# Kernel tuning notes

Measured on AMD Instinct MI355X. Metric: run time of the kernel, lower is better.

Reference implementation:

```python
import jax, jax.numpy as jnp
import numpy as np

B, S, DIM = 1, 2048, 2048
H, KVH = 32, 8
D = DIM // H  # 64


def setup_inputs() -> dict:
    key = jax.random.key(0)
    ks = jax.random.split(key, 10)
    x = jax.random.normal(ks[0], (B, S, DIM), dtype=jnp.float32)
    # RoPE frequencies: theta=10000, per LLaMA
    inv_freq = 1.0 / (10000.0 ** (np.arange(0, D, 2, dtype=np.float32) / D))  # (D/2,)
    angles = np.arange(S, dtype=np.float32)[:, None] * inv_freq[None, :]      # (S, D/2)
    freqs_cos = jnp.asarray(np.cos(angles))
    freqs_sin = jnp.asarray(np.sin(angles))
    # causal mask (1,1,S,S), 1 = keep, 0 = masked
    mask = jnp.tril(jnp.ones((S, S), dtype=jnp.int32))[None, None, :, :]
    w = 0.02
    Wq = jax.random.normal(ks[1], (DIM, H * D), dtype=jnp.float32) * w
    bq = jnp.zeros((H * D,), dtype=jnp.float32)
    Wk = jax.random.normal(ks[2], (DIM, KVH * D), dtype=jnp.float32) * w
    bk = jnp.zeros((KVH * D,), dtype=jnp.float32)
    Wv = jax.random.normal(ks[3], (DIM, KVH * D), dtype=jnp.float32) * w
    bv = jnp.zeros((KVH * D,), dtype=jnp.float32)
    Wo = jax.random.normal(ks[4], (H * D, DIM), dtype=jnp.float32) * w
    bo = jnp.zeros((DIM,), dtype=jnp.float32)
    return {"x": x, "freqs_cos": freqs_cos, "freqs_sin": freqs_sin, "mask": mask,
            "Wq": Wq, "bq": bq, "Wk": Wk, "bk": bk, "Wv": Wv, "bv": bv, "Wo": Wo, "bo": bo}


def _rope(t, cos, sin):
    # t: (B, S, h, D) with D even; rotate consecutive pairs (real form of complex mult)
    tr = t.reshape(*t.shape[:-1], -1, 2)          # (B,S,h,D/2,2)
    c = cos[None, :, None, :]                     # (1,S,1,D/2)
    s = sin[None, :, None, :]
    o0 = tr[..., 0] * c - tr[..., 1] * s
    o1 = tr[..., 0] * s + tr[..., 1] * c
    return jnp.stack([o0, o1], axis=-1).reshape(t.shape)


def reference(x, freqs_cos, freqs_sin, mask, Wq, bq, Wk, bk, Wv, bv, Wo, bo):
    b, s, dim = x.shape
    scale = 1.0 / jnp.sqrt(jnp.asarray(D, dtype=x.dtype))
    q = (x @ Wq + bq).reshape(b, s, H, D)
    k = (x @ Wk + bk).reshape(b, s, KVH, D)
    v = (x @ Wv + bv).reshape(b, s, KVH, D)
    q = _rope(q, freqs_cos, freqs_sin)
    k = _rope(k, freqs_cos, freqs_sin)
    # GQA: repeat kv heads to match query heads
    rep = H // KVH
    k = jnp.repeat(k, rep, axis=2)
    v = jnp.repeat(v, rep, axis=2)
    # to (B, H, S, D)
    q = q.transpose(0, 2, 1, 3)
    k = k.transpose(0, 2, 1, 3)
    v = v.transpose(0, 2, 1, 3)
    scores = jnp.einsum('bhqd,bhkd->bhqk', q, k) * scale   # (B,H,S,S)
    neg = jnp.asarray(jnp.finfo(scores.dtype).min, dtype=scores.dtype)
    scores = jnp.where(mask == 0, neg, scores)
    attn = jax.nn.softmax(scores, axis=-1)
    out = jnp.einsum('bhqk,bhkd->bhqd', attn, v)            # (B,H,S,D)
    out = out.transpose(0, 2, 1, 3).reshape(b, s, H * D)
    return out @ Wo + bo
```

## Files before the change

kernel.cpp:

```cpp
#include <hip/hip_runtime.h>
#include <stdint.h>

#define S_LEN 2048
#define DIM   2048
#define NHEAD 32
#define KVHEAD 8
#define HDIM  64
#define NQKV  3072

typedef __attribute__((ext_vector_type(8))) __bf16 bf16x8;
typedef __attribute__((ext_vector_type(4))) float f32x4;
typedef __attribute__((ext_vector_type(8))) unsigned short u16x8;
typedef __attribute__((ext_vector_type(4))) unsigned int u32x4;

#if __has_builtin(__builtin_amdgcn_exp2f)
#define EXP2F(x) __builtin_amdgcn_exp2f(x)
#else
#define EXP2F(x) exp2f(x)
#endif

__device__ __forceinline__ unsigned short f2bf(float f) {
  unsigned u = __builtin_bit_cast(unsigned, f);
  unsigned r = (u + 0x7FFFu + ((u >> 16) & 1u)) >> 16;
  return (unsigned short)r;
}
__device__ __forceinline__ float bf2f(unsigned short h) {
  unsigned u = ((unsigned)h) << 16;
  return __builtin_bit_cast(float, u);
}

__device__ __forceinline__ void gl_lds16(const void* g, void* l) {
  __builtin_amdgcn_global_load_lds(
      (const __attribute__((address_space(1))) unsigned*)g,
      (__attribute__((address_space(3))) unsigned*)l, 16, 0, 0);
}

__global__ void prep_kernel(const float* __restrict__ x,
                            const float* __restrict__ bq,
                            const float* __restrict__ bk,
                            const float* __restrict__ bv,
                            const float* __restrict__ Wq,
                            const float* __restrict__ Wk,
                            const float* __restrict__ Wv,
                            const float* __restrict__ Wo,
                            unsigned short* __restrict__ xb,
                            unsigned short* __restrict__ WqkvT,
                            unsigned short* __restrict__ WoT,
                            float* __restrict__ bqkv) {
  int idx = blockIdx.x;
  int tid = threadIdx.x;
  if (idx < 10240) {
    __shared__ float t[32][33];
    int bx = idx >> 6, by = idx & 63;
    const float* src; int C, sc, dbase; unsigned short* dst;
    if (bx < 64)      { src = Wq; C = 2048; sc = bx * 32;        dst = WqkvT; dbase = sc; }
    else if (bx < 80) { src = Wk; C = 512;  sc = (bx - 64) * 32; dst = WqkvT; dbase = 2048 + sc; }
    else if (bx < 96) { src = Wv; C = 512;  sc = (bx - 80) * 32; dst = WqkvT; dbase = 2560 + sc; }
    else              { src = Wo; C = 2048; sc = (bx - 96) * 32; dst = WoT;   dbase = sc; }
    int tx = tid & 31, ty = tid >> 5;
#pragma unroll
    for (int j = 0; j < 32; j += 8)
      t[ty + j][tx] = src[(size_t)(by * 32 + ty + j) * C + sc + tx];
    __syncthreads();
#pragma unroll
    for (int j = 0; j < 32; j += 8)
      dst[(size_t)(dbase + ty + j) * 2048 + by * 32 + tx] = f2bf(t[tx][ty + j]);
  } else if (idx < 14336) {
    int i = (idx - 10240) * 256 + tid;
    float4 v = ((const float4*)x)[i];
    ushort4 o;
    o.x = f2bf(v.x); o.y = f2bf(v.y); o.z = f2bf(v.z); o.w = f2bf(v.w);
    ((ushort4*)xb)[i] = o;
  } else {
    int i = (idx - 14336) * 256 + tid;
    if (i < NQKV)
      bqkv[i] = (i < 2048) ? bq[i] : (i < 2560 ? bk[i - 2048] : bv[i - 2560]);
  }
}

__global__ void rope_vt_kernel(unsigned short* __restrict__ qkv,
                               const float* __restrict__ fc,
                               const float* __restrict__ fs,
                               unsigned short* __restrict__ VT) {
  int idx = blockIdx.x;
  int tid = threadIdx.x;
  if (idx < 10240) {
    int i = idx * 256 + tid;
    int row = i / 1280;
    int p   = i - row * 1280;
    int col = (p < 1024) ? (p * 2) : (2048 + (p - 1024) * 2);
    int fi = p & 31;
    float c  = fc[row * 32 + fi];
    float sn = fs[row * 32 + fi];
    unsigned* base = (unsigned*)(qkv + (size_t)row * NQKV + col);
    unsigned v = *base;
    float x0 = bf2f((unsigned short)(v & 0xFFFF));
    float x1 = bf2f((unsigned short)(v >> 16));
    unsigned short o0 = f2bf(x0 * c - x1 * sn);
    unsigned short o1 = f2bf(x0 * sn + x1 * c);
    *base = (unsigned)o0 | ((unsigned)o1 << 16);
  } else {
    __shared__ unsigned short t[32][33];
    int sub = idx - 10240;
    int bx = (sub & 15) * 32;
    int by = (sub >> 4) * 32;
    int tx = tid & 31, ty = tid >> 5;
    const unsigned short* src = qkv + 2560;
#pragma unroll
    for (int j = 0; j < 32; j += 8)
      t[ty + j][tx] = src[(size_t)(by + ty + j) * 3072 + bx + tx];
    __syncthreads();
#pragma unroll
    for (int j = 0; j < 32; j += 8)
      VT[(size_t)(bx + ty + j) * 2048 + by + tx] = t[tx][ty + j];
  }
}

template <int OUT_BF16>
__global__ __launch_bounds__(512) void gemm_bt_kernel(
    const unsigned short* __restrict__ A,
    const unsigned short* __restrict__ BT,
    const float* __restrict__ bias,
    void* __restrict__ Cc, int M, int N, int K) {
  __shared__ char smem[65536];
  const int tid = threadIdx.x;
  const int lane = tid & 63;
  const int wid = tid >> 6;
  const int kh = wid >> 2;
  const int wsub = wid & 3;
  const int wm = wsub >> 1, wn = wsub & 1;
  const int rowA0 = blockIdx.x * 128;
  const int rowB0 = blockIdx.y * 128;
  const int l15 = lane & 15, l4 = lane >> 4;
  const int kcol = kh * 64 + l4 * 16;

  f32x4 acc[4][4];
#pragma unroll
  for (int i = 0; i < 4; i++)
#pragma unroll
    for (int j = 0; j < 4; j++) acc[i][j] = (f32x4){0.f, 0.f, 0.f, 0.f};

  const int nK = K >> 6;

  auto stage = [&](int buf, int kt) {
    const char* Ab = (const char*)A + ((size_t)rowA0 * K + (size_t)kt * 64) * 2;
    const char* Bb = (const char*)BT + ((size_t)rowB0 * K + (size_t)kt * 64) * 2;
#pragma unroll
    for (int h = 0; h < 2; ++h) {
      int o = h * 8192 + tid * 16;
      int r = o >> 7;
      int cb = (o & 127) ^ ((r & 7) << 4);
      gl_lds16(Ab + (size_t)r * (K * 2) + cb, smem + buf * 16384 + o);
      gl_lds16(Bb + (size_t)r * (K * 2) + cb, smem + 32768 + buf * 16384 + o);
    }
  };

  stage(0, 0);
  __syncthreads();
  int buf = 0;

  for (int kt = 0; kt < nK; ++kt) {
    if (kt + 1 < nK) stage(buf ^ 1, kt + 1);

    bf16x8 af[4], bfr[4];
#pragma unroll
    for (int i = 0; i < 4; i++) {
      int ra = wm * 64 + i * 16 + l15;
      int rb = wn * 64 + i * 16 + l15;
      af[i]  = *(const bf16x8*)(smem + buf * 16384 + ra * 128 + (kcol ^ ((ra & 7) << 4)));
      bfr[i] = *(const bf16x8*)(smem + 32768 + buf * 16384 + rb * 128 + (kcol ^ ((rb & 7) << 4)));
    }
#pragma unroll
    for (int i = 0; i < 4; i++)
#pragma unroll
      for (int j = 0; j < 4; j++)
        acc[i][j] = __builtin_amdgcn_mfma_f32_16x16x32_bf16(af[i], bfr[j], acc[i][j], 0, 0, 0);
    __syncthreads();
    buf ^= 1;
  }

  f32x4* eps = (f32x4*)smem;
  if (kh == 1) {
#pragma unroll
    for (int i = 0; i < 4; i++)
#pragma unroll
      for (int j = 0; j < 4; j++)
        eps[wsub * 1024 + (i * 4 + j) * 64 + lane] = acc[i][j];
  }
  __syncthreads();
  if (kh == 0) {
#pragma unroll
    for (int i = 0; i < 4; i++) {
      int row0 = rowA0 + wm * 64 + i * 16 + l4 * 4;
#pragma unroll
      for (int j = 0; j < 4; j++) {
        f32x4 oth = eps[wsub * 1024 + (i * 4 + j) * 64 + lane];
        int col = rowB0 + wn * 64 + j * 16 + l15;
        float bv_ = bias[col];
#pragma unroll
        for (int r = 0; r < 4; r++) {
          float v = acc[i][j][r] + oth[r] + bv_;
          size_t idx = (size_t)(row0 + r) * N + col;
          if (OUT_BF16) ((unsigned short*)Cc)[idx] = f2bf(v);
          else          ((float*)Cc)[idx] = v;
        }
      }
    }
  }
}

__global__ __launch_bounds__(512) void attn_kernel(
    const unsigned short* __restrict__ qkv,
    const unsigned short* __restrict__ VT,
    unsigned short* __restrict__ O) {
  __shared__ unsigned short Ks[3][64 * 64];
  __shared__ unsigned short VTs[3][64 * 64];

  const int tid = threadIdx.x;
  const int lane = tid & 63;
  const int w = tid >> 6;
  const int l15 = lane & 15, l4 = lane >> 4;
  const int kvh = blockIdx.x >> 5;
  const int pr  = blockIdx.x & 31;
  const int h = kvh * 4 + (w >> 1);
  const int qsub = (w & 1) * 16;

  auto issue = [&](int buf, int t) {
    int kvb = t * 64;
    int o = tid << 4;
    int r = o >> 7;
    int cb = (o & 127) ^ ((r & 7) << 4);
    gl_lds16((const char*)qkv + ((size_t)(kvb + r) * NQKV + 2048 + kvh * 64) * 2 + cb,
             (char*)&Ks[buf][0] + o);
    gl_lds16((const char*)VT + ((size_t)(kvh * 64 + r) * S_LEN + kvb) * 2 + cb,
             (char*)&VTs[buf][0] + o);
  };

#pragma unroll 1
  for (int ph = 0; ph < 2; ++ph) {
    const int qt = ph ? pr : 63 - pr;
    const int nt = (qt >> 1) + 1;
    const int qbase = qt * 32;

    bf16x8 qf[2];
    {
      const unsigned short* qrow = qkv + (size_t)(qbase + qsub + l15) * NQKV + h * 64;
#pragma unroll
      for (int kf = 0; kf < 2; ++kf) {
        u16x8 raw = *(const u16x8*)(qrow + kf * 32 + l4 * 8);
        u16x8 sc;
#pragma unroll
        for (int i = 0; i < 8; i++) sc[i] = f2bf(bf2f(raw[i]) * 0.1803368801111f);
        qf[kf] = __builtin_bit_cast(bf16x8, sc);
      }
    }

    f32x4 oacc[4];
    float lsum = 0.f;
#pragma unroll
    for (int d = 0; d < 4; d++) oacc[d] = (f32x4){0.f, 0.f, 0.f, 0.f};

    __syncthreads();
    issue(0, 0);
    if (nt > 1) issue(1, 1);

    for (int t = 0; t < nt; ++t) {
      if (t + 1 < nt) { asm volatile("s_waitcnt vmcnt(2)" ::: "memory"); }
      else            { asm volatile("s_waitcnt vmcnt(0)" ::: "memory"); }
      __builtin_amdgcn_s_barrier();
      asm volatile("" ::: "memory");
      if (t + 2 < nt) issue((t + 2) % 3, t + 2);
      const int buf = t % 3;

      f32x4 sacc[4];
#pragma unroll
      for (int nf = 0; nf < 4; nf++) sacc[nf] = (f32x4){0.f, 0.f, 0.f, 0.f};
#pragma unroll
      for (int nf = 0; nf < 4; nf++) {
#pragma unroll
        for (int kf = 0; kf < 2; kf++) {
          int row = nf * 16 + l15;
          bf16x8 kb = *(const bf16x8*)((const char*)&Ks[buf][0] + row * 128 +
                                       ((kf * 64 + l4 * 16) ^ ((row & 7) << 4)));
          sacc[nf] = __builtin_amdgcn_mfma_f32_16x16x32_bf16(kb, qf[kf], sacc[nf], 0, 0, 0);
        }
      }

      if (t == nt - 1) {
        int kvb = t * 64;
        int qpos = qbase + qsub + l15;
#pragma unroll
        for (int nf = 0; nf < 4; nf++) {
#pragma unroll
          for (int r = 0; r < 4; r++) {
            int kvpos = kvb + nf * 16 + l4 * 4 + r;
            if (kvpos > qpos) sacc[nf][r] = -3.0e38f;
          }
        }
      }

#pragma unroll
      for (int nf = 0; nf < 4; nf++) {
#pragma unroll
        for (int r = 0; r < 4; r++) {
          float p = EXP2F(sacc[nf][r]);
          lsum += p;
          sacc[nf][r] = p;
        }
      }

      unsigned wds[4][2];
#pragma unroll
      for (int nf = 0; nf < 4; nf++)
#pragma unroll
        for (int m = 0; m < 2; m++)
          asm("v_cvt_pk_bf16_f32 %0, %1, %2"
              : "=v"(wds[nf][m]) : "v"(sacc[nf][2 * m]), "v"(sacc[nf][2 * m + 1]));

      bf16x8 paf[2];
#pragma unroll
      for (int kc = 0; kc < 2; kc++) {
        unsigned a0 = wds[2 * kc][0], b0 = wds[2 * kc + 1][0];
        unsigned a1 = wds[2 * kc][1], b1 = wds[2 * kc + 1][1];
        asm("v_permlane32_swap_b32 %0, %1" : "+v"(a0), "+v"(b0));
        asm("v_permlane16_swap_b32 %0, %1" : "+v"(a0), "+v"(b0));
        asm("v_permlane32_swap_b32 %0, %1" : "+v"(a1), "+v"(b1));
        asm("v_permlane16_swap_b32 %0, %1" : "+v"(a1), "+v"(b1));
        u32x4 afu = (u32x4){a0, a1, b0, b1};
        paf[kc] = __builtin_bit_cast(bf16x8, afu);
      }

#pragma unroll
      for (int kc = 0; kc < 2; kc++) {
#pragma unroll
        for (int df = 0; df < 4; df++) {
          int row = df * 16 + l15;
          bf16x8 vb = *(const bf16x8*)((const char*)&VTs[buf][0] + row * 128 +
                                       ((kc * 64 + l4 * 16) ^ ((row & 7) << 4)));
          oacc[df] = __builtin_amdgcn_mfma_f32_16x16x32_bf16(paf[kc], vb, oacc[df], 0, 0, 0);
        }
      }
    }

    lsum += __shfl_xor(lsum, 16, 64);
    lsum += __shfl_xor(lsum, 32, 64);

#pragma unroll
    for (int r = 0; r < 4; r++) {
      float inv = 1.0f / __shfl(lsum, l4 * 4 + r, 16);
      int qpos = qbase + qsub + l4 * 4 + r;
#pragma unroll
      for (int df = 0; df < 4; df++)
        O[(size_t)qpos * DIM + h * 64 + df * 16 + l15] = f2bf(oacc[df][r] * inv);
    }
  }
}

extern "C" void kernel_launch(void* const* d_in, const int* in_sizes, int n_in,
                              void* d_out, int out_size, void* d_ws, size_t ws_size,
                              hipStream_t stream) {
  const float* x  = (const float*)d_in[0];
  const float* fc = (const float*)d_in[1];
  const float* fs = (const float*)d_in[2];
  const float* Wq = (const float*)d_in[4];
  const float* bq = (const float*)d_in[5];
  const float* Wk = (const float*)d_in[6];
  const float* bk = (const float*)d_in[7];
  const float* Wv = (const float*)d_in[8];
  const float* bv = (const float*)d_in[9];
  const float* Wo = (const float*)d_in[10];
  const float* bo = (const float*)d_in[11];
  float* out = (float*)d_out;

  char* ws = (char*)d_ws;
  unsigned short* xb    = (unsigned short*)(ws + 0);
  unsigned short* WqkvT = (unsigned short*)(ws + 8388608);
  unsigned short* WoT   = (unsigned short*)(ws + 20971520);
  float*          bqkv  = (float*)(ws + 29360128);
  unsigned short* qkv   = (unsigned short*)(ws + 29372416);
  unsigned short* VT    = WqkvT;
  unsigned short* attn  = xb;

  prep_kernel<<<14348, 256, 0, stream>>>(x, bq, bk, bv, Wq, Wk, Wv, Wo,
                                         xb, WqkvT, WoT, bqkv);
  gemm_bt_kernel<1><<<dim3(16, 24), 512, 0, stream>>>(xb, WqkvT, bqkv, qkv, 2048, 3072, 2048);
  rope_vt_kernel<<<11264, 256, 0, stream>>>(qkv, fc, fs, VT);
  attn_kernel<<<256, 512, 0, stream>>>(qkv, VT, attn);
  gemm_bt_kernel<0><<<dim3(16, 16), 512, 0, stream>>>(attn, WoT, bo, out, 2048, 2048, 2048);
}
```

Measured before the change: 228.0 us.

## Shrink GEMM N-tiles and split attention into one q-tile per block

The GEMM kernel now takes a template N-tile width: 96 columns for the QKV projection and 64 for the output projection. This gives a 16x32 grid in both cases, so more blocks spread across the many CUs. The attention kernel no longer pairs a long and a short q-tile per block; it launches 512 blocks, one q-tile each, ordered longest first, and adds s_setprio around the MFMA sections. It also sets launch_bounds occupancy hints. The costs are lower operand reuse per block, more blocks to schedule, and load balance in attention that now depends on the hardware scheduler.

After: 223.4 us. -2.0%, faster.

```diff
diff --git a/kernel.cpp b/kernel.cpp
--- a/kernel.cpp
+++ b/kernel.cpp
@@ -116,13 +116,14 @@
   }
 }
 
-template <int OUT_BF16>
-__global__ __launch_bounds__(512) void gemm_bt_kernel(
+template <int NJ, int OUT_BF16>
+__global__ __launch_bounds__(512, 4) void gemm_bt_kernel(
     const unsigned short* __restrict__ A,
     const unsigned short* __restrict__ BT,
     const float* __restrict__ bias,
     void* __restrict__ Cc, int M, int N, int K) {
-  __shared__ char smem[65536];
+  constexpr int BUFB = 16384 + NJ * 4096;
+  __shared__ char smem[2 * BUFB];
   const int tid = threadIdx.x;
   const int lane = tid & 63;
   const int wid = tid >> 6;
@@ -130,28 +131,39 @@
   const int wsub = wid & 3;
   const int wm = wsub >> 1, wn = wsub & 1;
   const int rowA0 = blockIdx.x * 128;
-  const int rowB0 = blockIdx.y * 128;
+  const int rowB0 = blockIdx.y * (32 * NJ);
   const int l15 = lane & 15, l4 = lane >> 4;
   const int kcol = kh * 64 + l4 * 16;
 
-  f32x4 acc[4][4];
+  f32x4 acc[4][NJ];
 #pragma unroll
   for (int i = 0; i < 4; i++)
 #pragma unroll
-    for (int j = 0; j < 4; j++) acc[i][j] = (f32x4){0.f, 0.f, 0.f, 0.f};
+    for (int j = 0; j < NJ; j++) acc[i][j] = (f32x4){0.f, 0.f, 0.f, 0.f};
 
   const int nK = K >> 6;
 
   auto stage = [&](int buf, int kt) {
     const char* Ab = (const char*)A + ((size_t)rowA0 * K + (size_t)kt * 64) * 2;
     const char* Bb = (const char*)BT + ((size_t)rowB0 * K + (size_t)kt * 64) * 2;
-#pragma unroll
-    for (int h = 0; h < 2; ++h) {
-      int o = h * 8192 + tid * 16;
+    char* Sb = smem + buf * BUFB;
+#pragma unroll
+    for (int j = 0; j < 2; ++j) {
+      int chunk = wid + 8 * j;
+      int o = chunk * 1024 + lane * 16;
       int r = o >> 7;
       int cb = (o & 127) ^ ((r & 7) << 4);
-      gl_lds16(Ab + (size_t)r * (K * 2) + cb, smem + buf * 16384 + o);
-      gl_lds16(Bb + (size_t)r * (K * 2) + cb, smem + 32768 + buf * 16384 + o);
+      gl_lds16(Ab + (size_t)r * (K * 2) + cb, Sb + chunk * 1024);
+    }
+#pragma unroll
+    for (int j = 0; j < (NJ + 1) / 2; ++j) {
+      int chunk = wid + 8 * j;
+      if (chunk < 4 * NJ) {
+        int o = chunk * 1024 + lane * 16;
+        int r = o >> 7;
+        int cb = (o & 127) ^ ((r & 7) << 4);
+        gl_lds16(Bb + (size_t)r * (K * 2) + cb, Sb + 16384 + chunk * 1024);
+      }
     }
   };
 
@@ -162,18 +174,22 @@
   for (int kt = 0; kt < nK; ++kt) {
     if (kt + 1 < nK) stage(buf ^ 1, kt + 1);
 
-    bf16x8 af[4], bfr[4];
+    bf16x8 af[4], bfr[NJ];
+    char* Sb = smem + buf * BUFB;
 #pragma unroll
     for (int i = 0; i < 4; i++) {
       int ra = wm * 64 + i * 16 + l15;
-      int rb = wn * 64 + i * 16 + l15;
-      af[i]  = *(const bf16x8*)(smem + buf * 16384 + ra * 128 + (kcol ^ ((ra & 7) << 4)));
-      bfr[i] = *(const bf16x8*)(smem + 32768 + buf * 16384 + rb * 128 + (kcol ^ ((rb & 7) << 4)));
+      af[i] = *(const bf16x8*)(Sb + ra * 128 + (kcol ^ ((ra & 7) << 4)));
+    }
+#pragma unroll
+    for (int j = 0; j < NJ; j++) {
+      int rb = wn * (NJ * 16) + j * 16 + l15;
+      bfr[j] = *(const bf16x8*)(Sb + 16384 + rb * 128 + (kcol ^ ((rb & 7) << 4)));
     }
 #pragma unroll
     for (int i = 0; i < 4; i++)
 #pragma unroll
-      for (int j = 0; j < 4; j++)
+      for (int j = 0; j < NJ; j++)
         acc[i][j] = __builtin_amdgcn_mfma_f32_16x16x32_bf16(af[i], bfr[j], acc[i][j], 0, 0, 0);
     __syncthreads();
     buf ^= 1;
@@ -184,8 +200,8 @@
 #pragma unroll
     for (int i = 0; i < 4; i++)
 #pragma unroll
-      for (int j = 0; j < 4; j++)
-        eps[wsub * 1024 + (i * 4 + j) * 64 + lane] = acc[i][j];
+      for (int j = 0; j < NJ; j++)
+        eps[wsub * (4 * NJ * 64) + (i * NJ + j) * 64 + lane] = acc[i][j];
   }
   __syncthreads();
   if (kh == 0) {
@@ -193,9 +209,9 @@
     for (int i = 0; i < 4; i++) {
       int row0 = rowA0 + wm * 64 + i * 16 + l4 * 4;
 #pragma unroll
-      for (int j = 0; j < 4; j++) {
-        f32x4 oth = eps[wsub * 1024 + (i * 4 + j) * 64 + lane];
-        int col = rowB0 + wn * 64 + j * 16 + l15;
+      for (int j = 0; j < NJ; j++) {
+        f32x4 oth = eps[wsub * (4 * NJ * 64) + (i * NJ + j) * 64 + lane];
+        int col = rowB0 + wn * (NJ * 16) + j * 16 + l15;
         float bv_ = bias[col];
 #pragma unroll
         for (int r = 0; r < 4; r++) {
@@ -209,7 +225,7 @@
   }
 }
 
-__global__ __launch_bounds__(512) void attn_kernel(
+__global__ __launch_bounds__(512, 4) void attn_kernel(
     const unsigned short* __restrict__ qkv,
     const unsigned short* __restrict__ VT,
     unsigned short* __restrict__ O) {
@@ -220,10 +236,12 @@
   const int lane = tid & 63;
   const int w = tid >> 6;
   const int l15 = lane & 15, l4 = lane >> 4;
-  const int kvh = blockIdx.x >> 5;
-  const int pr  = blockIdx.x & 31;
+  const int kvh = blockIdx.x & 7;
+  const int qt  = 63 - (blockIdx.x >> 3);
   const int h = kvh * 4 + (w >> 1);
   const int qsub = (w & 1) * 16;
+  const int nt = (qt >> 1) + 1;
+  const int qbase = qt * 32;
 
   auto issue = [&](int buf, int t) {
     int kvb = t * 64;
@@ -236,123 +254,119 @@
              (char*)&VTs[buf][0] + o);
   };
 
-#pragma unroll 1
-  for (int ph = 0; ph < 2; ++ph) {
-    const int qt = ph ? pr : 63 - pr;
-    const int nt = (qt >> 1) + 1;
-    const int qbase = qt * 32;
-
-    bf16x8 qf[2];
-    {
-      const unsigned short* qrow = qkv + (size_t)(qbase + qsub + l15) * NQKV + h * 64;
-#pragma unroll
-      for (int kf = 0; kf < 2; ++kf) {
-        u16x8 raw = *(const u16x8*)(qrow + kf * 32 + l4 * 8);
-        u16x8 sc;
-#pragma unroll
-        for (int i = 0; i < 8; i++) sc[i] = f2bf(bf2f(raw[i]) * 0.1803368801111f);
-        qf[kf] = __builtin_bit_cast(bf16x8, sc);
-      }
-    }
-
-    f32x4 oacc[4];
-    float lsum = 0.f;
-#pragma unroll
-    for (int d = 0; d < 4; d++) oacc[d] = (f32x4){0.f, 0.f, 0.f, 0.f};
-
-    __syncthreads();
-    issue(0, 0);
-    if (nt > 1) issue(1, 1);
-
-    for (int t = 0; t < nt; ++t) {
-      if (t + 1 < nt) { asm volatile("s_waitcnt vmcnt(2)" ::: "memory"); }
-      else            { asm volatile("s_waitcnt vmcnt(0)" ::: "memory"); }
-      __builtin_amdgcn_s_barrier();
-      asm volatile("" ::: "memory");
-      if (t + 2 < nt) issue((t + 2) % 3, t + 2);
-      const int buf = t % 3;
-
-      f32x4 sacc[4];
-#pragma unroll
-      for (int nf = 0; nf < 4; nf++) sacc[nf] = (f32x4){0.f, 0.f, 0.f, 0.f};
+  bf16x8 qf[2];
+  {
+    const unsigned short* qrow = qkv + (size_t)(qbase + qsub + l15) * NQKV + h * 64;
+#pragma unroll
+    for (int kf = 0; kf < 2; ++kf) {
+      u16x8 raw = *(const u16x8*)(qrow + kf * 32 + l4 * 8);
+      u16x8 sc;
+#pragma unroll
+      for (int i = 0; i < 8; i++) sc[i] = f2bf(bf2f(raw[i]) * 0.1803368801111f);
+      qf[kf] = __builtin_bit_cast(bf16x8, sc);
+    }
+  }
+
+  f32x4 oacc[4];
+  float lsum = 0.f;
+#pragma unroll
+  for (int d = 0; d < 4; d++) oacc[d] = (f32x4){0.f, 0.f, 0.f, 0.f};
+
+  issue(0, 0);
+  if (nt > 1) issue(1, 1);
+
+  for (int t = 0; t < nt; ++t) {
+    if (t + 1 < nt) { asm volatile("s_waitcnt vmcnt(2)" ::: "memory"); }
+    else            { asm volatile("s_waitcnt vmcnt(0)" ::: "memory"); }
+    __builtin_amdgcn_s_barrier();
+    asm volatile("" ::: "memory");
+    if (t + 2 < nt) issue((t + 2) % 3, t + 2);
+    const int buf = t % 3;
+
+    f32x4 sacc[4];
+#pragma unroll
+    for (int nf = 0; nf < 4; nf++) sacc[nf] = (f32x4){0.f, 0.f, 0.f, 0.f};
+    __builtin_amdgcn_s_setprio(1);
+#pragma unroll
+    for (int nf = 0; nf < 4; nf++) {
+#pragma unroll
+      for (int kf = 0; kf < 2; kf++) {
+        int row = nf * 16 + l15;
+        bf16x8 kb = *(const bf16x8*)((const char*)&Ks[buf][0] + row * 128 +
+                                     ((kf * 64 + l4 * 16) ^ ((row & 7) << 4)));
+        sacc[nf] = __builtin_amdgcn_mfma_f32_16x16x32_bf16(kb, qf[kf], sacc[nf], 0, 0, 0);
+      }
+    }
+    __builtin_amdgcn_s_setprio(0);
+
+    if (t == nt - 1) {
+      int kvb = t * 64;
+      int qpos = qbase + qsub + l15;
 #pragma unroll
       for (int nf = 0; nf < 4; nf++) {
 #pragma unroll
-        for (int kf = 0; kf < 2; kf++) {
-          int row = nf * 16 + l15;
-          bf16x8 kb = *(const bf16x8*)((const char*)&Ks[buf][0] + row * 128 +
-                                       ((kf * 64 + l4 * 16) ^ ((row & 7) << 4)));
-          sacc[nf] = __builtin_amdgcn_mfma_f32_16x16x32_bf16(kb, qf[kf], sacc[nf], 0, 0, 0);
+        for (int r = 0; r < 4; r++) {
+          int kvpos = kvb + nf * 16 + l4 * 4 + r;
+          if (kvpos > qpos) sacc[nf][r] = -3.0e38f;
         }
       }
-
-      if (t == nt - 1) {
-        int kvb = t * 64;
-        int qpos = qbase + qsub + l15;
-#pragma unroll
-        for (int nf = 0; nf < 4; nf++) {
-#pragma unroll
-          for (int r = 0; r < 4; r++) {
-            int kvpos = kvb + nf * 16 + l4 * 4 + r;
-            if (kvpos > qpos) sacc[nf][r] = -3.0e38f;
-          }
-        }
-      }
-
-#pragma unroll
-      for (int nf = 0; nf < 4; nf++) {
-#pragma unroll
-        for (int r = 0; r < 4; r++) {
-          float p = EXP2F(sacc[nf][r]);
-          lsum += p;
-          sacc[nf][r] = p;
-        }
-      }
-
-      unsigned wds[4][2];
-#pragma unroll
-      for (int nf = 0; nf < 4; nf++)
-#pragma unroll
-        for (int m = 0; m < 2; m++)
-          asm("v_cvt_pk_bf16_f32 %0, %1, %2"
-              : "=v"(wds[nf][m]) : "v"(sacc[nf][2 * m]), "v"(sacc[nf][2 * m + 1]));
-
-      bf16x8 paf[2];
-#pragma unroll
-      for (int kc = 0; kc < 2; kc++) {
-        unsigned a0 = wds[2 * kc][0], b0 = wds[2 * kc + 1][0];
-        unsigned a1 = wds[2 * kc][1], b1 = wds[2 * kc + 1][1];
-        asm("v_permlane32_swap_b32 %0, %1" : "+v"(a0), "+v"(b0));
-        asm("v_permlane16_swap_b32 %0, %1" : "+v"(a0), "+v"(b0));
-        asm("v_permlane32_swap_b32 %0, %1" : "+v"(a1), "+v"(b1));
-        asm("v_permlane16_swap_b32 %0, %1" : "+v"(a1), "+v"(b1));
-        u32x4 afu = (u32x4){a0, a1, b0, b1};
-        paf[kc] = __builtin_bit_cast(bf16x8, afu);
-      }
-
-#pragma unroll
-      for (int kc = 0; kc < 2; kc++) {
-#pragma unroll
-        for (int df = 0; df < 4; df++) {
-          int row = df * 16 + l15;
-          bf16x8 vb = *(const bf16x8*)((const char*)&VTs[buf][0] + row * 128 +
-                                       ((kc * 64 + l4 * 16) ^ ((row & 7) << 4)));
-          oacc[df] = __builtin_amdgcn_mfma_f32_16x16x32_bf16(paf[kc], vb, oacc[df], 0, 0, 0);
-        }
-      }
-    }
-
-    lsum += __shfl_xor(lsum, 16, 64);
-    lsum += __shfl_xor(lsum, 32, 64);
-
-#pragma unroll
-    for (int r = 0; r < 4; r++) {
-      float inv = 1.0f / __shfl(lsum, l4 * 4 + r, 16);
-      int qpos = qbase + qsub + l4 * 4 + r;
-#pragma unroll
-      for (int df = 0; df < 4; df++)
-        O[(size_t)qpos * DIM + h * 64 + df * 16 + l15] = f2bf(oacc[df][r] * inv);
-    }
+    }
+
+#pragma unroll
+    for (int nf = 0; nf < 4; nf++) {
+#pragma unroll
+      for (int r = 0; r < 4; r++) {
+        float p = EXP2F(sacc[nf][r]);
+        lsum += p;
+        sacc[nf][r] = p;
+      }
+    }
+
+    unsigned wds[4][2];
+#pragma unroll
+    for (int nf = 0; nf < 4; nf++)
+#pragma unroll
+      for (int m = 0; m < 2; m++)
+        asm("v_cvt_pk_bf16_f32 %0, %1, %2"
+            : "=v"(wds[nf][m]) : "v"(sacc[nf][2 * m]), "v"(sacc[nf][2 * m + 1]));
+
+    bf16x8 paf[2];
+#pragma unroll
+    for (int kc = 0; kc < 2; kc++) {
+      unsigned a0 = wds[2 * kc][0], b0 = wds[2 * kc + 1][0];
+      unsigned a1 = wds[2 * kc][1], b1 = wds[2 * kc + 1][1];
+      asm("v_permlane32_swap_b32 %0, %1" : "+v"(a0), "+v"(b0));
+      asm("v_permlane16_swap_b32 %0, %1" : "+v"(a0), "+v"(b0));
+      asm("v_permlane32_swap_b32 %0, %1" : "+v"(a1), "+v"(b1));
+      asm("v_permlane16_swap_b32 %0, %1" : "+v"(a1), "+v"(b1));
+      u32x4 afu = (u32x4){a0, a1, b0, b1};
+      paf[kc] = __builtin_bit_cast(bf16x8, afu);
+    }
+
+    __builtin_amdgcn_s_setprio(1);
+#pragma unroll
+    for (int kc = 0; kc < 2; kc++) {
+#pragma unroll
+      for (int df = 0; df < 4; df++) {
+        int row = df * 16 + l15;
+        bf16x8 vb = *(const bf16x8*)((const char*)&VTs[buf][0] + row * 128 +
+                                     ((kc * 64 + l4 * 16) ^ ((row & 7) << 4)));
+        oacc[df] = __builtin_amdgcn_mfma_f32_16x16x32_bf16(paf[kc], vb, oacc[df], 0, 0, 0);
+      }
+    }
+    __builtin_amdgcn_s_setprio(0);
+  }
+
+  lsum += __shfl_xor(lsum, 16, 64);
+  lsum += __shfl_xor(lsum, 32, 64);
+
+#pragma unroll
+  for (int r = 0; r < 4; r++) {
+    float inv = 1.0f / __shfl(lsum, l4 * 4 + r, 16);
+    int qpos = qbase + qsub + l4 * 4 + r;
+#pragma unroll
+    for (int df = 0; df < 4; df++)
+      O[(size_t)qpos * DIM + h * 64 + df * 16 + l15] = f2bf(oacc[df][r] * inv);
   }
 }
 
@@ -383,8 +397,8 @@
 
   prep_kernel<<<14348, 256, 0, stream>>>(x, bq, bk, bv, Wq, Wk, Wv, Wo,
                                          xb, WqkvT, WoT, bqkv);
-  gemm_bt_kernel<1><<<dim3(16, 24), 512, 0, stream>>>(xb, WqkvT, bqkv, qkv, 2048, 3072, 2048);
+  gemm_bt_kernel<3, 1><<<dim3(16, 32), 512, 0, stream>>>(xb, WqkvT, bqkv, qkv, 2048, 3072, 2048);
   rope_vt_kernel<<<11264, 256, 0, stream>>>(qkv, fc, fs, VT);
-  attn_kernel<<<256, 512, 0, stream>>>(qkv, VT, attn);
-  gemm_bt_kernel<0><<<dim3(16, 16), 512, 0, stream>>>(attn, WoT, bo, out, 2048, 2048, 2048);
-}
+  attn_kernel<<<512, 512, 0, stream>>>(qkv, VT, attn);
+  gemm_bt_kernel<2, 0><<<dim3(16, 32), 512, 0, stream>>>(attn, WoT, bo, out, 2048, 2048, 2048);
+}
```
